# Performance work log

Hardware: AMD Instinct MI355X
Metric: run time of the kernel (lower is better)

Reference implementation:

```python
import math
import jax, jax.numpy as jnp
import numpy as np

B, S, D, H = 4, 2048, 1024, 16
DK = D // H
THETA = 10000.0


def _rope(xh, pos):
    # xh: [B, H, S, DK], pos: [S]
    half = jnp.arange(0, DK, 2, dtype=jnp.float32) / DK
    inv_freq = THETA ** (-half)                      # [DK/2]
    ang = pos.astype(jnp.float32)[:, None] * inv_freq  # [S, DK/2]
    cos, sin = jnp.cos(ang).astype(xh.dtype), jnp.sin(ang).astype(xh.dtype)
    x1, x2 = xh[..., 0::2], xh[..., 1::2]
    r1 = x1 * cos - x2 * sin
    r2 = x1 * sin + x2 * cos
    return jnp.stack([r1, r2], axis=-1).reshape(xh.shape)


def setup_inputs() -> dict:
    key = jax.random.key(0)
    kx, kq, kk, kv, ko = jax.random.split(key, 5)
    std = 0.02
    x = jax.random.normal(kx, (B, S, D), jnp.float32)
    wq = jax.random.normal(kq, (D, D), jnp.float32) * std
    wk = jax.random.normal(kk, (D, D), jnp.float32) * std
    wv = jax.random.normal(kv, (D, D), jnp.float32) * std
    wo = jax.random.normal(ko, (D, D), jnp.float32) * std
    token_positions = jnp.arange(S, dtype=jnp.int32)
    return {"x": x, "wq": wq, "wk": wk, "wv": wv, "wo": wo,
            "token_positions": token_positions}


def reference(x, wq, wk, wv, wo, token_positions):
    # bias-free linear projections: y = x @ W^T (torch Linear convention)
    q = x @ wq.T
    k = x @ wk.T
    v = x @ wv.T
    # split heads: [B, S, D] -> [B, H, S, DK]
    to_heads = lambda t: t.reshape(B, S, H, DK).transpose(0, 2, 1, 3)
    qh, kh, vh = to_heads(q), to_heads(k), to_heads(v)
    qh = _rope(qh, token_positions)
    kh = _rope(kh, token_positions)
    scores = jnp.einsum('bhqd,bhkd->bhqk', qh, kh) / math.sqrt(DK)
    causal = jnp.tril(jnp.ones((S, S), dtype=bool))
    scores = jnp.where(causal, scores, -jnp.inf)
    attn = jax.nn.softmax(scores, axis=-1)
    out = jnp.einsum('bhqk,bhkd->bhqd', attn, vh)       # [B, H, S, DK]
    out = out.transpose(0, 2, 1, 3).reshape(B, S, D)    # merge heads
    return out @ wo.T
```

## Files before the change

kernel.cpp:

```cpp
#include <hip/hip_runtime.h>

#define B_ 4
#define S_ 2048
#define D_ 1024
#define H_ 16
#define DK_ 64
#define M_ (B_*S_)
#define K_ D_
#define N_ D_

typedef unsigned short u16;
typedef unsigned int u32;
typedef __bf16 bf16x8 __attribute__((ext_vector_type(8)));
typedef float f32x4 __attribute__((ext_vector_type(4)));
typedef u32 u32x4v __attribute__((ext_vector_type(4)));

#define EXP2F(x) __builtin_amdgcn_exp2f(x)

__device__ __forceinline__ u16 f2bf(float f) {
    u32 u = __builtin_bit_cast(u32, f);
    u += 0x7fff + ((u >> 16) & 1);
    return (u16)(u >> 16);
}
__device__ __forceinline__ float bf2f(u16 h) {
    u32 u = ((u32)h) << 16;
    return __builtin_bit_cast(float, u);
}
__device__ __forceinline__ u32 pack_trunc(float a, float b) {
    return (__builtin_bit_cast(u32, a) >> 16) | (__builtin_bit_cast(u32, b) & 0xffff0000u);
}

#define GLDS16(g, l) __builtin_amdgcn_global_load_lds( \
    (__attribute__((address_space(1))) void*)(g),      \
    (__attribute__((address_space(3))) void*)(l), 16, 0, 0)

__global__ __launch_bounds__(256) void cvt_x(const float* __restrict__ in,
                                             u16* __restrict__ out, int n4) {
    const int i = blockIdx.x * 256 + threadIdx.x;
    if (i >= n4) return;
    const float4 f = *(const float4*)(in + (size_t)i * 4);
    u32 p0 = (u32)f2bf(f.x) | ((u32)f2bf(f.y) << 16);
    u32 p1 = (u32)f2bf(f.z) | ((u32)f2bf(f.w) << 16);
    *(uint2*)(out + (size_t)i * 4) = make_uint2(p0, p1);
}

__global__ __launch_bounds__(256) void cvt_w4(
    const float* __restrict__ w0, const float* __restrict__ w1,
    const float* __restrict__ w2, const float* __restrict__ w3,
    u16* __restrict__ o0, u16* __restrict__ o1,
    u16* __restrict__ o2, u16* __restrict__ o3) {
    const int wi = blockIdx.y;
    const float* in = (wi == 0) ? w0 : (wi == 1) ? w1 : (wi == 2) ? w2 : w3;
    u16* out       = (wi == 0) ? o0 : (wi == 1) ? o1 : (wi == 2) ? o2 : o3;
    const int i = blockIdx.x * 256 + threadIdx.x;
    const float4 f = *(const float4*)(in + (size_t)i * 4);
    u32 p0 = (u32)f2bf(f.x) | ((u32)f2bf(f.y) << 16);
    u32 p1 = (u32)f2bf(f.z) | ((u32)f2bf(f.w) << 16);
    *(uint2*)(out + (size_t)i * 4) = make_uint2(p0, p1);
}

template <int MODE>
__device__ __forceinline__ void gemm_tile(const u16* __restrict__ A,
                                          const u16* __restrict__ Bm,
                                          void* __restrict__ Cv) {
    __shared__ u16 As[128 * 32];
    __shared__ u16 Bs[128 * 32];
    const int tid  = threadIdx.x;
    const int wave = tid >> 6, lane = tid & 63;
    const int m0 = blockIdx.y * 128, n0 = blockIdx.x * 128;
    const int wm = wave & 1, wn = wave >> 1;
    const int quad = lane >> 4, mcol = lane & 15;

    const int c0 = wave, c1 = wave + 4;
    const int r0 = c0 * 16 + (lane >> 2), r1 = c1 * 16 + (lane >> 2);
    const int kb = (lane & 3) * 8;
    const u16* ga0 = A  + (size_t)(m0 + r0) * K_ + kb;
    const u16* ga1 = A  + (size_t)(m0 + r1) * K_ + kb;
    const u16* gb0 = Bm + (size_t)(n0 + r0) * K_ + kb;
    const u16* gb1 = Bm + (size_t)(n0 + r1) * K_ + kb;
    u16* la0 = &As[c0 * 512];
    u16* la1 = &As[c1 * 512];
    u16* lb0 = &Bs[c0 * 512];
    u16* lb1 = &Bs[c1 * 512];

    f32x4 acc[4][4];
#pragma unroll
    for (int i = 0; i < 4; i++)
#pragma unroll
        for (int j = 0; j < 4; j++) acc[i][j] = f32x4{0.f, 0.f, 0.f, 0.f};

    for (int kt = 0; kt < K_; kt += 32) {
        __syncthreads();
        GLDS16(ga0, la0); GLDS16(ga1, la1);
        GLDS16(gb0, lb0); GLDS16(gb1, lb1);
        ga0 += 32; ga1 += 32; gb0 += 32; gb1 += 32;
        __syncthreads();

        bf16x8 af[4], bfr[4];
#pragma unroll
        for (int i = 0; i < 4; i++) {
            af[i]  = *(const bf16x8*)&As[(size_t)(wm * 64 + i * 16 + mcol) * 32 + quad * 8];
            bfr[i] = *(const bf16x8*)&Bs[(size_t)(wn * 64 + i * 16 + mcol) * 32 + quad * 8];
        }
#pragma unroll
        for (int i = 0; i < 4; i++)
#pragma unroll
            for (int j = 0; j < 4; j++)
                acc[i][j] = __builtin_amdgcn_mfma_f32_16x16x32_bf16(
                    af[i], bfr[j], acc[i][j], 0, 0, 0);
    }

#pragma unroll
    for (int i = 0; i < 4; i++) {
        const int row = m0 + wm * 64 + i * 16 + quad * 4;
#pragma unroll
        for (int j = 0; j < 4; j++) {
            const int col = n0 + wn * 64 + j * 16 + mcol;
            if constexpr (MODE == 2) {
                const int hh = col >> 6, dd = col & 63;
                const int bb = row >> 11, ss = row & 2047;
                const u32 lo = (u32)f2bf(acc[i][j][0]) | ((u32)f2bf(acc[i][j][1]) << 16);
                const u32 hi = (u32)f2bf(acc[i][j][2]) | ((u32)f2bf(acc[i][j][3]) << 16);
                *(uint2*)((u16*)Cv + ((size_t)((bb * H_ + hh) * DK_ + dd)) * S_ + ss) =
                    make_uint2(lo, hi);
            } else {
#pragma unroll
                for (int r = 0; r < 4; r++) {
                    if constexpr (MODE == 1)
                        ((float*)Cv)[(size_t)(row + r) * N_ + col] = acc[i][j][r];
                    else
                        ((u16*)Cv)[(size_t)(row + r) * N_ + col] = f2bf(acc[i][j][r]);
                }
            }
        }
    }
}

__global__ __launch_bounds__(256) void gemm_qk_kernel(
    const u16* __restrict__ x,
    const u16* __restrict__ wq, const u16* __restrict__ wk,
    u16* __restrict__ q, u16* __restrict__ k) {
    const u16* Bm = (blockIdx.z == 0) ? wq : wk;
    u16* C        = (blockIdx.z == 0) ? q  : k;
    gemm_tile<0>(x, Bm, C);
}

__global__ __launch_bounds__(256) void gemm_v_kernel(
    const u16* __restrict__ x, const u16* __restrict__ wv, u16* __restrict__ vt) {
    gemm_tile<2>(x, wv, vt);
}

__global__ __launch_bounds__(256) void gemm_out_kernel(
    const u16* __restrict__ o, const u16* __restrict__ wo, float* __restrict__ out) {
    gemm_tile<1>(o, wo, out);
}

__global__ __launch_bounds__(256) void rope_qk(u16* __restrict__ q,
                                               u16* __restrict__ k,
                                               const int* __restrict__ pos) {
    const int idx = blockIdx.x * 256 + threadIdx.x;
    const int i = idx & 31;
    const int h = (idx >> 5) & (H_ - 1);
    const int s = (idx >> 9) & (S_ - 1);
    const int b = idx >> 20;
    const float p = (float)pos[s];
    const float inv = exp2f((float)i * (-13.287712379549449f / 32.f));
    const float ang = p * inv;
    float sn, cs;
    __sincosf(ang, &sn, &cs);
    const float QSC = 0.18033688011112042f;
    const size_t off = ((size_t)(b * S_ + s)) * D_ + h * DK_ + 2 * i;
    {
        float x1 = bf2f(q[off]), x2 = bf2f(q[off + 1]);
        q[off]     = f2bf((x1 * cs - x2 * sn) * QSC);
        q[off + 1] = f2bf((x1 * sn + x2 * cs) * QSC);
    }
    {
        float x1 = bf2f(k[off]), x2 = bf2f(k[off + 1]);
        k[off]     = f2bf(x1 * cs - x2 * sn);
        k[off + 1] = f2bf(x1 * sn + x2 * cs);
    }
}

__global__ __launch_bounds__(256) void attn_kernel(
    const u16* __restrict__ q, const u16* __restrict__ k,
    const u16* __restrict__ vt, u16* __restrict__ o) {
    __shared__ u16 Ks[64 * 64];
    __shared__ u16 Vs[64 * 64];

    const int tid = threadIdx.x, wave = tid >> 6, lane = tid & 63;
    const int flat = blockIdx.x;
    const int qp = flat >> 6;
    const int h = flat & (H_ - 1);
    const int b = (flat >> 4) & 3;
    const int quad = lane >> 4, mcol = lane & 15;
    const int srd = mcol & 7;

    const int rr2 = tid >> 2, cc2 = tid & 3;
    const int sw = rr2 & 7;
    const int so0 = rr2 * 64 + (((cc2 * 2)     ^ sw) << 3);
    const int so1 = rr2 * 64 + (((cc2 * 2 + 1) ^ sw) << 3);
    const int prr = (rr2 & 35) | ((rr2 & 12) << 1) | ((rr2 & 16) >> 2);
    const int ch2 = cc2 * 16;
    const u16* krow = k + ((size_t)(b * S_ + prr)) * D_ + h * DK_ + ch2;
    const u16* vrow = vt + ((size_t)((b * H_ + h) * DK_ + rr2)) * S_ + ch2;

    for (int pass = 0; pass < 2; pass++) {
        const int qt = pass ? (15 - qp) : qp;
        const int q0 = qt * 128;
        const int wq0 = q0 + wave * 32;
        const int jmax = 2 * qt + 1;

        bf16x8 qf[2][2];
#pragma unroll
        for (int g = 0; g < 2; g++) {
            const u16* qs = q + ((size_t)(b * S_ + wq0 + g * 16 + mcol)) * D_ + h * DK_ + quad * 8;
            qf[g][0] = *(const bf16x8*)qs;
            qf[g][1] = *(const bf16x8*)(qs + 32);
        }

        float m[2] = {-1e30f, -1e30f}, l[2] = {0.f, 0.f};
        f32x4 oacc[2][4];
#pragma unroll
        for (int g = 0; g < 2; g++)
#pragma unroll
            for (int dn = 0; dn < 4; dn++) oacc[g][dn] = f32x4{0.f, 0.f, 0.f, 0.f};

        uint4 kr0 = *(const uint4*)(krow);
        uint4 kr1 = *(const uint4*)(krow + 8);
        uint4 vr0 = *(const uint4*)(vrow);
        uint4 vr1 = *(const uint4*)(vrow + 8);

        for (int j = 0; j <= jmax; j++) {
            __syncthreads();
            *(uint4*)&Ks[so0] = kr0;
            *(uint4*)&Ks[so1] = kr1;
            *(uint4*)&Vs[so0] = vr0;
            *(uint4*)&Vs[so1] = vr1;
            __syncthreads();

            if (j < jmax) {
                kr0 = *(const uint4*)(krow + (size_t)(j + 1) * 64 * D_);
                kr1 = *(const uint4*)(krow + (size_t)(j + 1) * 64 * D_ + 8);
                vr0 = *(const uint4*)(vrow + (j + 1) * 64);
                vr1 = *(const uint4*)(vrow + (j + 1) * 64 + 8);
            }

            if (j * 64 > wq0 + 31) continue;

            f32x4 st[2][4];
            __builtin_amdgcn_s_setprio(1);
#pragma unroll
            for (int n = 0; n < 4; n++) {
                const u16* kl = &Ks[(n * 16 + mcol) * 64];
                bf16x8 kf0 = *(const bf16x8*)&kl[(quad ^ srd) << 3];
                bf16x8 kf1 = *(const bf16x8*)&kl[((quad | 4) ^ srd) << 3];
                f32x4 z0 = f32x4{0.f, 0.f, 0.f, 0.f};
                z0 = __builtin_amdgcn_mfma_f32_16x16x32_bf16(kf0, qf[0][0], z0, 0, 0, 0);
                z0 = __builtin_amdgcn_mfma_f32_16x16x32_bf16(kf1, qf[0][1], z0, 0, 0, 0);
                st[0][n] = z0;
                f32x4 z1 = f32x4{0.f, 0.f, 0.f, 0.f};
                z1 = __builtin_amdgcn_mfma_f32_16x16x32_bf16(kf0, qf[1][0], z1, 0, 0, 0);
                z1 = __builtin_amdgcn_mfma_f32_16x16x32_bf16(kf1, qf[1][1], z1, 0, 0, 0);
                st[1][n] = z1;
            }
            __builtin_amdgcn_s_setprio(0);

            if (j * 64 + 63 > wq0) {
#pragma unroll
                for (int g = 0; g < 2; g++) {
                    const int qg = wq0 + g * 16 + mcol;
#pragma unroll
                    for (int n = 0; n < 4; n++) {
                        const int tb = j * 64 + ((n >> 1) << 5) + ((n & 1) << 2) + quad * 8;
#pragma unroll
                        for (int r = 0; r < 4; r++)
                            if (tb + r > qg) st[g][n][r] = -1e30f;
                    }
                }
            }

#pragma unroll
            for (int g = 0; g < 2; g++) {
                float mx = st[g][0][0];
#pragma unroll
                for (int n = 0; n < 4; n++)
#pragma unroll
                    for (int r = 0; r < 4; r++) mx = fmaxf(mx, st[g][n][r]);
                mx = fmaxf(mx, __shfl_xor(mx, 16));
                mx = fmaxf(mx, __shfl_xor(mx, 32));
                float al = 1.f;
                const bool need = !__all(mx <= m[g] + 8.f);
                if (need) {
                    const float mnew = fmaxf(m[g], mx);
                    al = EXP2F(m[g] - mnew);
                    m[g] = mnew;
                }
                float sum = 0.f;
#pragma unroll
                for (int n = 0; n < 4; n++)
#pragma unroll
                    for (int r = 0; r < 4; r++) {
                        const float p = EXP2F(st[g][n][r] - m[g]);
                        st[g][n][r] = p;
                        sum += p;
                    }
                sum += __shfl_xor(sum, 16);
                sum += __shfl_xor(sum, 32);
                l[g] = l[g] * al + sum;
                if (need) {
                    float alphaT[4];
#pragma unroll
                    for (int r = 0; r < 4; r++) alphaT[r] = __shfl(al, quad * 4 + r);
#pragma unroll
                    for (int dn = 0; dn < 4; dn++)
#pragma unroll
                        for (int r = 0; r < 4; r++) oacc[g][dn][r] *= alphaT[r];
                }
            }

            bf16x8 pf[2][2];
#pragma unroll
            for (int g = 0; g < 2; g++) {
                u32x4v w0, w1;
                w0[0] = pack_trunc(st[g][0][0], st[g][0][1]);
                w0[1] = pack_trunc(st[g][0][2], st[g][0][3]);
                w0[2] = pack_trunc(st[g][1][0], st[g][1][1]);
                w0[3] = pack_trunc(st[g][1][2], st[g][1][3]);
                w1[0] = pack_trunc(st[g][2][0], st[g][2][1]);
                w1[1] = pack_trunc(st[g][2][2], st[g][2][3]);
                w1[2] = pack_trunc(st[g][3][0], st[g][3][1]);
                w1[3] = pack_trunc(st[g][3][2], st[g][3][3]);
                pf[g][0] = __builtin_bit_cast(bf16x8, w0);
                pf[g][1] = __builtin_bit_cast(bf16x8, w1);
            }

            __builtin_amdgcn_s_setprio(1);
#pragma unroll
            for (int dn = 0; dn < 4; dn++) {
                const u16* vl = &Vs[(dn * 16 + mcol) * 64];
                bf16x8 vf0 = *(const bf16x8*)&vl[(quad ^ srd) << 3];
                bf16x8 vf1 = *(const bf16x8*)&vl[((quad | 4) ^ srd) << 3];
#pragma unroll
                for (int g = 0; g < 2; g++) {
                    oacc[g][dn] = __builtin_amdgcn_mfma_f32_16x16x32_bf16(pf[g][0], vf0, oacc[g][dn], 0, 0, 0);
                    oacc[g][dn] = __builtin_amdgcn_mfma_f32_16x16x32_bf16(pf[g][1], vf1, oacc[g][dn], 0, 0, 0);
                }
            }
            __builtin_amdgcn_s_setprio(0);
        }

#pragma unroll
        for (int g = 0; g < 2; g++) {
            float linv[4];
#pragma unroll
            for (int r = 0; r < 4; r++) linv[r] = 1.f / __shfl(l[g], quad * 4 + r);
#pragma unroll
            for (int dn = 0; dn < 4; dn++)
#pragma unroll
                for (int r = 0; r < 4; r++) {
                    const int row = wq0 + g * 16 + quad * 4 + r;
                    o[((size_t)(b * S_ + row)) * D_ + h * DK_ + dn * 16 + mcol] =
                        f2bf(oacc[g][dn][r] * linv[r]);
                }
        }
    }
}

extern "C" void kernel_launch(void* const* d_in, const int* in_sizes, int n_in,
                              void* d_out, int out_size, void* d_ws, size_t ws_size,
                              hipStream_t stream) {
    const float* x  = (const float*)d_in[0];
    const float* wq = (const float*)d_in[1];
    const float* wk = (const float*)d_in[2];
    const float* wv = (const float*)d_in[3];
    const float* wo = (const float*)d_in[4];
    const int*   tp = (const int*)d_in[5];
    float* out = (float*)d_out;

    u16* ws = (u16*)d_ws;
    const size_t NE = (size_t)M_ * D_;
    const size_t WE = (size_t)N_ * K_;
    u16* xb  = ws;
    u16* wqb = ws + NE;
    u16* wkb = wqb + WE;
    u16* wvb = wkb + WE;
    u16* wob = wvb + WE;
    u16* qb  = wob + WE;
    u16* kb  = qb + NE;
    u16* vtb = (u16*)d_out;
    u16* ob  = xb;

    dim3 blk(256);
    cvt_x<<<dim3((int)(NE / 1024)), blk, 0, stream>>>(x, xb, (int)(NE / 4));
    cvt_w4<<<dim3((int)(WE / 1024), 4), blk, 0, stream>>>(wq, wk, wv, wo, wqb, wkb, wvb, wob);

    gemm_qk_kernel<<<dim3(N_ / 128, M_ / 128, 2), blk, 0, stream>>>(xb, wqb, wkb, qb, kb);
    gemm_v_kernel<<<dim3(N_ / 128, M_ / 128, 1), blk, 0, stream>>>(xb, wvb, vtb);
    rope_qk<<<dim3((B_ * S_ * H_ * 32) / 256), blk, 0, stream>>>(qb, kb, tp);
    attn_kernel<<<dim3((S_ / 128 / 2) * H_ * B_), blk, 0, stream>>>(qb, kb, vtb, ob);
    gemm_out_kernel<<<dim3(N_ / 128, M_ / 128, 1), blk, 0, stream>>>(ob, wob, out);
}
```

Before: 287.0 us.

## Double-buffer GEMM LDS tiles, merge QKV launches, vectorize RoPE

```diff
diff --git a/kernel.cpp b/kernel.cpp
--- a/kernel.cpp
+++ b/kernel.cpp
@@ -63,8 +63,8 @@
 __device__ __forceinline__ void gemm_tile(const u16* __restrict__ A,
                                           const u16* __restrict__ Bm,
                                           void* __restrict__ Cv) {
-    __shared__ u16 As[128 * 32];
-    __shared__ u16 Bs[128 * 32];
+    __shared__ u16 As[2][128 * 32];
+    __shared__ u16 Bs[2][128 * 32];
     const int tid  = threadIdx.x;
     const int wave = tid >> 6, lane = tid & 63;
     const int m0 = blockIdx.y * 128, n0 = blockIdx.x * 128;
@@ -78,10 +78,7 @@
     const u16* ga1 = A  + (size_t)(m0 + r1) * K_ + kb;
     const u16* gb0 = Bm + (size_t)(n0 + r0) * K_ + kb;
     const u16* gb1 = Bm + (size_t)(n0 + r1) * K_ + kb;
-    u16* la0 = &As[c0 * 512];
-    u16* la1 = &As[c1 * 512];
-    u16* lb0 = &Bs[c0 * 512];
-    u16* lb1 = &Bs[c1 * 512];
+    const int lo0 = c0 * 512, lo1 = c1 * 512;
 
     f32x4 acc[4][4];
 #pragma unroll
@@ -89,18 +86,25 @@
 #pragma unroll
         for (int j = 0; j < 4; j++) acc[i][j] = f32x4{0.f, 0.f, 0.f, 0.f};
 
+    GLDS16(ga0, &As[0][lo0]); GLDS16(ga1, &As[0][lo1]);
+    GLDS16(gb0, &Bs[0][lo0]); GLDS16(gb1, &Bs[0][lo1]);
+    ga0 += 32; ga1 += 32; gb0 += 32; gb1 += 32;
+    __syncthreads();
+
     for (int kt = 0; kt < K_; kt += 32) {
-        __syncthreads();
-        GLDS16(ga0, la0); GLDS16(ga1, la1);
-        GLDS16(gb0, lb0); GLDS16(gb1, lb1);
-        ga0 += 32; ga1 += 32; gb0 += 32; gb1 += 32;
-        __syncthreads();
+        const int cur = (kt >> 5) & 1;
+        if (kt + 32 < K_) {
+            const int nxt = cur ^ 1;
+            GLDS16(ga0, &As[nxt][lo0]); GLDS16(ga1, &As[nxt][lo1]);
+            GLDS16(gb0, &Bs[nxt][lo0]); GLDS16(gb1, &Bs[nxt][lo1]);
+            ga0 += 32; ga1 += 32; gb0 += 32; gb1 += 32;
+        }
 
         bf16x8 af[4], bfr[4];
 #pragma unroll
         for (int i = 0; i < 4; i++) {
-            af[i]  = *(const bf16x8*)&As[(size_t)(wm * 64 + i * 16 + mcol) * 32 + quad * 8];
-            bfr[i] = *(const bf16x8*)&Bs[(size_t)(wn * 64 + i * 16 + mcol) * 32 + quad * 8];
+            af[i]  = *(const bf16x8*)&As[cur][(wm * 64 + i * 16 + mcol) * 32 + quad * 8];
+            bfr[i] = *(const bf16x8*)&Bs[cur][(wn * 64 + i * 16 + mcol) * 32 + quad * 8];
         }
 #pragma unroll
         for (int i = 0; i < 4; i++)
@@ -108,6 +112,8 @@
             for (int j = 0; j < 4; j++)
                 acc[i][j] = __builtin_amdgcn_mfma_f32_16x16x32_bf16(
                     af[i], bfr[j], acc[i][j], 0, 0, 0);
+
+        __syncthreads();
     }
 
 #pragma unroll
@@ -136,18 +142,18 @@
     }
 }
 
-__global__ __launch_bounds__(256) void gemm_qk_kernel(
+__global__ __launch_bounds__(256) void gemm_qkv_kernel(
     const u16* __restrict__ x,
     const u16* __restrict__ wq, const u16* __restrict__ wk,
-    u16* __restrict__ q, u16* __restrict__ k) {
-    const u16* Bm = (blockIdx.z == 0) ? wq : wk;
-    u16* C        = (blockIdx.z == 0) ? q  : k;
-    gemm_tile<0>(x, Bm, C);
-}
-
-__global__ __launch_bounds__(256) void gemm_v_kernel(
-    const u16* __restrict__ x, const u16* __restrict__ wv, u16* __restrict__ vt) {
-    gemm_tile<2>(x, wv, vt);
+    const u16* __restrict__ wv,
+    u16* __restrict__ q, u16* __restrict__ k, u16* __restrict__ vt) {
+    if (blockIdx.z == 2) {
+        gemm_tile<2>(x, wv, vt);
+    } else {
+        const u16* Bm = blockIdx.z ? wk : wq;
+        u16* C        = blockIdx.z ? k  : q;
+        gemm_tile<0>(x, Bm, C);
+    }
 }
 
 __global__ __launch_bounds__(256) void gemm_out_kernel(
@@ -159,27 +165,43 @@
                                                u16* __restrict__ k,
                                                const int* __restrict__ pos) {
     const int idx = blockIdx.x * 256 + threadIdx.x;
-    const int i = idx & 31;
-    const int h = (idx >> 5) & (H_ - 1);
-    const int s = (idx >> 9) & (S_ - 1);
-    const int b = idx >> 20;
+    const int seg = idx & 3;
+    const int h = (idx >> 2) & (H_ - 1);
+    const int s = (idx >> 6) & (S_ - 1);
+    const int b = idx >> 17;
     const float p = (float)pos[s];
-    const float inv = exp2f((float)i * (-13.287712379549449f / 32.f));
-    const float ang = p * inv;
-    float sn, cs;
-    __sincosf(ang, &sn, &cs);
     const float QSC = 0.18033688011112042f;
-    const size_t off = ((size_t)(b * S_ + s)) * D_ + h * DK_ + 2 * i;
-    {
-        float x1 = bf2f(q[off]), x2 = bf2f(q[off + 1]);
-        q[off]     = f2bf((x1 * cs - x2 * sn) * QSC);
-        q[off + 1] = f2bf((x1 * sn + x2 * cs) * QSC);
+    const size_t off = ((size_t)(b * S_ + s)) * D_ + h * DK_ + seg * 16;
+
+    u32 qa[8], ka[8];
+    *(uint4*)&qa[0] = *(const uint4*)(q + off);
+    *(uint4*)&qa[4] = *(const uint4*)(q + off + 8);
+    *(uint4*)&ka[0] = *(const uint4*)(k + off);
+    *(uint4*)&ka[4] = *(const uint4*)(k + off + 8);
+#pragma unroll
+    for (int w = 0; w < 8; w++) {
+        const int i = seg * 8 + w;
+        const float inv = exp2f((float)i * (-13.287712379549449f / 32.f));
+        const float ang = p * inv;
+        float sn, cs;
+        __sincosf(ang, &sn, &cs);
+        {
+            const float x1 = bf2f((u16)(qa[w] & 0xffff));
+            const float x2 = bf2f((u16)(qa[w] >> 16));
+            qa[w] = (u32)f2bf((x1 * cs - x2 * sn) * QSC) |
+                    ((u32)f2bf((x1 * sn + x2 * cs) * QSC) << 16);
+        }
+        {
+            const float x1 = bf2f((u16)(ka[w] & 0xffff));
+            const float x2 = bf2f((u16)(ka[w] >> 16));
+            ka[w] = (u32)f2bf(x1 * cs - x2 * sn) |
+                    ((u32)f2bf(x1 * sn + x2 * cs) << 16);
+        }
     }
-    {
-        float x1 = bf2f(k[off]), x2 = bf2f(k[off + 1]);
-        k[off]     = f2bf(x1 * cs - x2 * sn);
-        k[off + 1] = f2bf(x1 * sn + x2 * cs);
-    }
+    *(uint4*)(q + off)     = *(uint4*)&qa[0];
+    *(uint4*)(q + off + 8) = *(uint4*)&qa[4];
+    *(uint4*)(k + off)     = *(uint4*)&ka[0];
+    *(uint4*)(k + off + 8) = *(uint4*)&ka[4];
 }
 
 __global__ __launch_bounds__(256) void attn_kernel(
@@ -395,9 +417,8 @@
     cvt_x<<<dim3((int)(NE / 1024)), blk, 0, stream>>>(x, xb, (int)(NE / 4));
     cvt_w4<<<dim3((int)(WE / 1024), 4), blk, 0, stream>>>(wq, wk, wv, wo, wqb, wkb, wvb, wob);
 
-    gemm_qk_kernel<<<dim3(N_ / 128, M_ / 128, 2), blk, 0, stream>>>(xb, wqb, wkb, qb, kb);
-    gemm_v_kernel<<<dim3(N_ / 128, M_ / 128, 1), blk, 0, stream>>>(xb, wvb, vtb);
-    rope_qk<<<dim3((B_ * S_ * H_ * 32) / 256), blk, 0, stream>>>(qb, kb, tp);
+    gemm_qkv_kernel<<<dim3(N_ / 128, M_ / 128, 3), blk, 0, stream>>>(xb, wqb, wkb, wvb, qb, kb, vtb);
+    rope_qk<<<dim3((B_ * S_ * H_ * 4) / 256), blk, 0, stream>>>(qb, kb, tp);
     attn_kernel<<<dim3((S_ / 128 / 2) * H_ * B_), blk, 0, stream>>>(qb, kb, vtb, ob);
     gemm_out_kernel<<<dim3(N_ / 128, M_ / 128, 1), blk, 0, stream>>>(ob, wob, out);
 }
```

New measurement: 275.6 us. 4.0% less time.
